# Optimization experiments

Measured on AMD Instinct MI355X. Metric: run time of the kernel, lower is better.

Reference implementation:

```python
import jax, jax.numpy as jnp
import numpy as np
import math

FACTOR = 5

def setup_inputs() -> dict:
    key = jax.random.key(0)
    k1, k2, k3, k4 = jax.random.split(key, 4)
    B, L, H, D = 4, 2048, 8, 64
    sample_k = FACTOR * math.ceil(math.log(L))  # 40
    queries = jax.random.normal(k1, (B, L, H, D), dtype=jnp.float32)
    keys = jax.random.normal(k2, (B, L, H, D), dtype=jnp.float32)
    values = jax.random.normal(k3, (B, L, H, D), dtype=jnp.float32)
    index_sample = jax.random.randint(k4, (L, sample_k), 0, L, dtype=jnp.int32)
    return {"queries": queries, "keys": keys, "values": values, "index_sample": index_sample}

def reference(queries, keys, values, index_sample):
    B, L_Q, H, D = queries.shape
    L_K = keys.shape[1]
    # [B,L,H,D] -> [B,H,L,D]
    Q = jnp.swapaxes(queries, 1, 2)
    K = jnp.swapaxes(keys, 1, 2)
    # values are cumsum'ed along the length axis before attention
    Vc = jnp.cumsum(jnp.swapaxes(values, 1, 2), axis=-2)
    u = min(FACTOR * math.ceil(math.log(L_Q)), L_Q)  # n_top
    # --- _prob_QK ---
    # gather sampled keys per query position: [B,H,L_Q,sample_k,D]
    K_sample = K[:, :, index_sample, :]
    # sampled scores: [B,H,L_Q,sample_k]
    Q_K_sample = jnp.einsum('bhqd,bhqsd->bhqs', Q, K_sample)
    # sparsity measure M = max - mean(scaled by L_K)
    M = Q_K_sample.max(axis=-1) - Q_K_sample.sum(axis=-1) / L_K  # [B,H,L_Q]
    M_top = jax.lax.top_k(M, u)[1]  # [B,H,u] query indices
    # gather top queries: [B,H,u,D]
    Q_reduce = jnp.take_along_axis(Q, M_top[..., None], axis=2)
    # full scores for selected queries: [B,H,u,L_K]
    scores = jnp.einsum('bhud,bhkd->bhuk', Q_reduce, K)
    scale = 1.0 / math.sqrt(D)
    scores = scores * scale
    # mask_flag=False, output_attention=False -> plain softmax then matmul with cumsum'ed V
    attn = jax.nn.softmax(scores, axis=-1)
    context = jnp.einsum('bhuk,bhkd->bhud', attn, Vc)  # [B,H,u,D]
    return context
```

## Files before the change

### kernel.cpp

```cpp
#include <hip/hip_runtime.h>
#include <hip/hip_bf16.h>
#include <math.h>

#define B 4
#define L 2048
#define H 8
#define D 64
#define SK 40
#define U 40
#define JC 32
#define JCL (L / JC)

#define OFF_M     0
#define OFF_TOP   262144
#define OFF_T     270336
#define OFF_PART  10756096
#define OFF_CSUM  21241856

__device__ __forceinline__ float dot4(float4 a, float4 b) {
    return fmaf(a.x, b.x, fmaf(a.y, b.y, fmaf(a.z, b.z, a.w * b.w)));
}

__global__ __launch_bounds__(256) void k_msamp(const float* __restrict__ Q,
                                               const float* __restrict__ K,
                                               const int* __restrict__ idx,
                                               float* __restrict__ M) {
    int g  = blockIdx.x & 7;
    int b  = g >> 1;
    int hh = g & 1;
    int t  = threadIdx.x;
    int wave = t >> 6;
    int lane = t & 63;
    int qp = lane >> 5;
    int hp = (lane >> 3) & 3;
    int c  = lane & 7;
    int h  = hh * 4 + hp;
    int q  = (blockIdx.x >> 3) * 8 + wave * 2 + qp;

    const float* qrow = Q + (size_t)((b * L + q) * H + h) * D + c * 8;
    float4 qa = *(const float4*)qrow;
    float4 qb = *(const float4*)(qrow + 4);

    int s1 = lane & 31;
    int v1 = idx[q * SK + s1];
    int s2 = 32 + s1; if (s2 > SK - 1) s2 = SK - 1;
    int v2 = idx[q * SK + s2];

    const float* kbase = K + (size_t)b * L * H * D + (size_t)h * D + c * 8;

    float vmax = -__builtin_inff();
    float vsum = 0.f;
#pragma unroll 8
    for (int s = 0; s < SK; ++s) {
        int kidx = (s < 32) ? __shfl(v1, qp * 32 + s, 64)
                            : __shfl(v2, qp * 32 + (s - 32), 64);
        const float* kp = kbase + (size_t)kidx * (H * D);
        float4 ka = *(const float4*)kp;
        float4 kb = *(const float4*)(kp + 4);
        float d8 = dot4(qa, ka) + dot4(qb, kb);
        d8 += __shfl_xor(d8, 1, 64);
        d8 += __shfl_xor(d8, 2, 64);
        d8 += __shfl_xor(d8, 4, 64);
        vmax = fmaxf(vmax, d8);
        vsum += d8;
    }
    if (c == 0) M[(size_t)(b * H + h) * L + q] = vmax - vsum * (1.0f / (float)L);
}

__global__ __launch_bounds__(256) void k_topk(const float* __restrict__ M,
                                              int* __restrict__ top) {
    __shared__ unsigned long long cand[L];
    __shared__ unsigned int bins[256];
    __shared__ unsigned int red[256];
    __shared__ int cnt2;

    int bh = blockIdx.x;
    int tid = threadIdx.x;
    const float* m = M + (size_t)bh * L;

    bins[tid] = 0;
    if (tid == 0) cnt2 = 0;

    const float4* m4 = (const float4*)(m + tid * 8);
    float4 fa = m4[0], fb = m4[1];
    float f8[8] = {fa.x, fa.y, fa.z, fa.w, fb.x, fb.y, fb.z, fb.w};
    unsigned int u8[8];
    unsigned int umin = 0xFFFFFFFFu, umax = 0u;
#pragma unroll
    for (int e = 0; e < 8; ++e) {
        unsigned int bits = __float_as_uint(f8[e]);
        unsigned int u = (bits & 0x80000000u) ? ~bits : (bits | 0x80000000u);
        u8[e] = u;
        umin = min(umin, u);
        umax = max(umax, u);
    }
    red[tid] = umin;
    __syncthreads();
    for (int s = 128; s; s >>= 1) {
        if (tid < s) red[tid] = min(red[tid], red[tid + s]);
        __syncthreads();
    }
    unsigned int kmin = red[0];
    __syncthreads();
    red[tid] = umax;
    __syncthreads();
    for (int s = 128; s; s >>= 1) {
        if (tid < s) red[tid] = max(red[tid], red[tid + s]);
        __syncthreads();
    }
    unsigned int kmax = red[0];
    __syncthreads();

    unsigned int range = kmax - kmin;
    if (range == 0u) {
        if (tid < U) top[bh * U + tid] = tid;
        return;
    }
    int hb = 31 - __clz(range);
    int shift = (hb > 7) ? (hb - 7) : 0;

#pragma unroll
    for (int e = 0; e < 8; ++e) {
        unsigned int bin = (u8[e] - kmin) >> shift;
        atomicAdd(&bins[bin], 1u);
    }
    __syncthreads();

    red[tid] = bins[tid];
    __syncthreads();
    for (int s = 1; s < 256; s <<= 1) {
        unsigned int add = (tid + s < 256) ? red[tid + s] : 0u;
        __syncthreads();
        red[tid] += add;
        __syncthreads();
    }
    int cnt = __syncthreads_count(red[tid] >= U);
    unsigned int t = (unsigned int)(cnt - 1);

#pragma unroll
    for (int e = 0; e < 8; ++e) {
        unsigned int u = u8[e];
        if (((u - kmin) >> shift) >= t) {
            int pos = atomicAdd(&cnt2, 1);
            int i = tid * 8 + e;
            cand[pos] = ((unsigned long long)u << 11) | (unsigned long long)(2047 - i);
        }
    }
    __syncthreads();
    int C = cnt2;

    for (int j = tid; j < C; j += 256) {
        unsigned long long kj = cand[j];
        int r = 0;
        for (int kk = 0; kk < C; ++kk) r += (cand[kk] > kj);
        if (r < U) top[bh * U + r] = 2047 - (int)(kj & 0x7FFull);
    }
}

__global__ __launch_bounds__(256) void k_scores(const float* __restrict__ Q,
                                                const float* __restrict__ K,
                                                const int* __restrict__ top,
                                                float* __restrict__ T,
                                                float* __restrict__ csum) {
    __shared__ float4 sQ4[U * 16];
    int bh = blockIdx.x >> 4;
    int kc = blockIdx.x & 15;
    int b = bh >> 3, h = bh & (H - 1);
    int tid = threadIdx.x;
    int lane = tid & 63;
    int w = tid >> 6;

    for (int i = tid; i < U * 16; i += 256) {
        int u = i >> 4, c = i & 15;
        int qidx = top[bh * U + u];
        sQ4[i] = *((const float4*)(Q + (size_t)((b * L + qidx) * H + h) * D) + c);
    }

    int k0 = kc * 128 + lane;
    const float4* kr0 = (const float4*)(K + (size_t)((b * L + k0) * H + h) * D);
    const float4* kr1 = (const float4*)(K + (size_t)((b * L + k0 + 64) * H + h) * D);
    float4 kv0[16], kv1[16];
#pragma unroll
    for (int i = 0; i < 16; ++i) { kv0[i] = kr0[i]; kv1[i] = kr1[i]; }
    __syncthreads();

    float* Tb = T + (size_t)bh * U * L;
    for (int uu = 0; uu < 10; ++uu) {
        int u = w * 10 + uu;
        float s0 = 0.f, s1 = 0.f;
#pragma unroll
        for (int i = 0; i < 16; ++i) {
            float4 q4 = sQ4[u * 16 + i];
            s0 += dot4(q4, kv0[i]);
            s1 += dot4(q4, kv1[i]);
        }
        float e0 = __expf(s0 * 0.125f);
        float e1 = __expf(s1 * 0.125f);
        Tb[(size_t)u * L + k0]      = e0;
        Tb[(size_t)u * L + k0 + 64] = e1;
        float c0 = e0, c1 = e1;
#pragma unroll
        for (int o = 1; o < 64; o <<= 1) {
            c0 += __shfl_xor(c0, o, 64);
            c1 += __shfl_xor(c1, o, 64);
        }
        if (lane == 0) {
            csum[((size_t)bh * U + u) * JC + 2 * kc]     = c0;
            csum[((size_t)bh * U + u) * JC + 2 * kc + 1] = c1;
        }
    }
}

__global__ __launch_bounds__(256) void k_ctx(const float* __restrict__ V,
                                             const float* __restrict__ E,
                                             const float* __restrict__ csum,
                                             float* __restrict__ part) {
    __shared__ float sT[U][JCL];
    int bh = blockIdx.x >> 5;
    int jc = blockIdx.x & 31;
    int b = bh >> 3, h = bh & (H - 1);
    int tid = threadIdx.x;
    int w = tid >> 6;
    int lane = tid & 63;
    int j2 = lane >> 4;
    int d4 = lane & 15;
    int jlane = lane & 31;

    const float* Eg = E + (size_t)bh * U * L + jc * JCL;
#pragma unroll
    for (int r = 0; r < 10; ++r) {
        int u = w * 10 + r;
        float cv = csum[((size_t)bh * U + u) * JC + jlane];
        float tv = (jlane > jc) ? cv : 0.f;
        tv += __shfl_xor(tv, 1, 64);
        tv += __shfl_xor(tv, 2, 64);
        tv += __shfl_xor(tv, 4, 64);
        tv += __shfl_xor(tv, 8, 64);
        tv += __shfl_xor(tv, 16, 64);
        float v = Eg[(size_t)u * L + lane];
#pragma unroll
        for (int s = 1; s < 64; s <<= 1) {
            float o = __shfl_down(v, s, 64);
            v += (lane + s < 64) ? o : 0.f;
        }
        sT[u][lane] = v + tv;
    }
    __syncthreads();

    float4 acc[10];
#pragma unroll
    for (int uu = 0; uu < 10; ++uu) acc[uu] = make_float4(0.f, 0.f, 0.f, 0.f);

    const float* Vb = V + (size_t)(b * L) * (H * D) + (size_t)h * D + d4 * 4;
#pragma unroll 4
    for (int it = 0; it < JCL / 4; ++it) {
        int j = it * 4 + j2;
        float4 v4 = *(const float4*)(Vb + (size_t)(jc * JCL + j) * (H * D));
#pragma unroll
        for (int uu = 0; uu < 10; ++uu) {
            float tj = sT[w * 10 + uu][j];
            acc[uu].x = fmaf(tj, v4.x, acc[uu].x);
            acc[uu].y = fmaf(tj, v4.y, acc[uu].y);
            acc[uu].z = fmaf(tj, v4.z, acc[uu].z);
            acc[uu].w = fmaf(tj, v4.w, acc[uu].w);
        }
    }

    float* po = part + ((size_t)jc * (B * H) + bh) * (U * D);
#pragma unroll
    for (int uu = 0; uu < 10; ++uu) {
        float4 a = acc[uu];
        a.x += __shfl_xor(a.x, 16, 64); a.y += __shfl_xor(a.y, 16, 64);
        a.z += __shfl_xor(a.z, 16, 64); a.w += __shfl_xor(a.w, 16, 64);
        a.x += __shfl_xor(a.x, 32, 64); a.y += __shfl_xor(a.y, 32, 64);
        a.z += __shfl_xor(a.z, 32, 64); a.w += __shfl_xor(a.w, 32, 64);
        if (j2 == 0) *(float4*)(po + (w * 10 + uu) * D + d4 * 4) = a;
    }
}

__global__ __launch_bounds__(256) void k_red(const float* __restrict__ part,
                                             const float* __restrict__ csum,
                                             float* __restrict__ out) {
    __shared__ float sden[4];
    int o = blockIdx.x * 256 + threadIdx.x;
    int bh = o / (U * D);
    int rest = o - bh * (U * D);
    int u = rest >> 6;
    int tid = threadIdx.x;
    int ubase = ((blockIdx.x * 256) % (U * D)) >> 6;

    if (tid < 128) {
        int ul = tid >> 5, j = tid & 31;
        float v = csum[((size_t)bh * U + ubase + ul) * JC + j];
        v += __shfl_xor(v, 1, 64);
        v += __shfl_xor(v, 2, 64);
        v += __shfl_xor(v, 4, 64);
        v += __shfl_xor(v, 8, 64);
        v += __shfl_xor(v, 16, 64);
        if (j == 0) sden[ul] = v;
    }
    __syncthreads();

    float s = 0.f;
#pragma unroll
    for (int jc = 0; jc < JC; ++jc)
        s += part[(size_t)(jc * (B * H) + bh) * (U * D) + rest];
    out[o] = s / sden[u - ubase];
}

extern "C" void kernel_launch(void* const* d_in, const int* in_sizes, int n_in,
                              void* d_out, int out_size, void* d_ws, size_t ws_size,
                              hipStream_t stream) {
    const float* Q  = (const float*)d_in[0];
    const float* K  = (const float*)d_in[1];
    const float* V  = (const float*)d_in[2];
    const int* idx  = (const int*)d_in[3];
    float* out = (float*)d_out;

    float* M    = (float*)((char*)d_ws + OFF_M);
    int*   top  = (int*)  ((char*)d_ws + OFF_TOP);
    float* T    = (float*)((char*)d_ws + OFF_T);
    float* part = (float*)((char*)d_ws + OFF_PART);
    float* csum = (float*)((char*)d_ws + OFF_CSUM);

    k_msamp<<<(L / 8) * 8, 256, 0, stream>>>(Q, K, idx, M);
    k_topk<<<B * H, 256, 0, stream>>>(M, top);
    k_scores<<<B * H * 16, 256, 0, stream>>>(Q, K, top, T, csum);
    k_ctx<<<B * H * JC, 256, 0, stream>>>(V, T, csum, part);
    k_red<<<(B * H * U * D) / 256, 256, 0, stream>>>(part, csum, out);
}
```

Before: 150.7 us.

## Fuse scores, context and reduction into one cooperative kernel with grid syncs

Replaces the three tail kernels (scores, context, reduce) with a single cooperative kernel of 256 blocks that runs each phase and separates them with grid-wide syncs. Each block now handles two key chunks per phase, and the context split is halved from 32 to 16 chunks, which shrinks the partial buffer and the final reduction. The aim is to remove launch gaps and cut partial-sum traffic. In exchange, grid sync adds its own cost, and the smaller grid gives less parallelism per phase. A fallback path launches the three phases as separate kernels if the cooperative launch fails.

```diff
diff --git a/kernel.cpp b/kernel.cpp
--- a/kernel.cpp
+++ b/kernel.cpp
@@ -1,6 +1,8 @@
 #include <hip/hip_runtime.h>
-#include <hip/hip_bf16.h>
+#include <hip/hip_cooperative_groups.h>
 #include <math.h>
+
+namespace cg = cooperative_groups;
 
 #define B 4
 #define L 2048
@@ -8,14 +10,15 @@
 #define D 64
 #define SK 40
 #define U 40
-#define JC 32
+#define JC 16
 #define JCL (L / JC)
+#define CSG 32
 
 #define OFF_M     0
 #define OFF_TOP   262144
 #define OFF_T     270336
 #define OFF_PART  10756096
-#define OFF_CSUM  21241856
+#define OFF_CSUM  15998976
 
 __device__ __forceinline__ float dot4(float4 a, float4 b) {
     return fmaf(a.x, b.x, fmaf(a.y, b.y, fmaf(a.z, b.z, a.w * b.w)));
@@ -157,155 +160,211 @@
     }
 }
 
-__global__ __launch_bounds__(256) void k_scores(const float* __restrict__ Q,
-                                                const float* __restrict__ K,
-                                                const int* __restrict__ top,
-                                                float* __restrict__ T,
-                                                float* __restrict__ csum) {
-    __shared__ float4 sQ4[U * 16];
-    int bh = blockIdx.x >> 4;
-    int kc = blockIdx.x & 15;
+
+__device__ __forceinline__ void phaseA(const float* __restrict__ Q,
+                                       const float* __restrict__ K,
+                                       const int* __restrict__ top,
+                                       float* __restrict__ T,
+                                       float* __restrict__ csum,
+                                       float4* sQ4) {
+    int tid = threadIdx.x, lane = tid & 63, w = tid >> 6;
+    int bh = blockIdx.x >> 3;
+    int kc2 = blockIdx.x & 7;
     int b = bh >> 3, h = bh & (H - 1);
-    int tid = threadIdx.x;
-    int lane = tid & 63;
-    int w = tid >> 6;
 
     for (int i = tid; i < U * 16; i += 256) {
         int u = i >> 4, c = i & 15;
         int qidx = top[bh * U + u];
         sQ4[i] = *((const float4*)(Q + (size_t)((b * L + qidx) * H + h) * D) + c);
     }
-
-    int k0 = kc * 128 + lane;
-    const float4* kr0 = (const float4*)(K + (size_t)((b * L + k0) * H + h) * D);
-    const float4* kr1 = (const float4*)(K + (size_t)((b * L + k0 + 64) * H + h) * D);
-    float4 kv0[16], kv1[16];
-#pragma unroll
-    for (int i = 0; i < 16; ++i) { kv0[i] = kr0[i]; kv1[i] = kr1[i]; }
     __syncthreads();
 
     float* Tb = T + (size_t)bh * U * L;
-    for (int uu = 0; uu < 10; ++uu) {
-        int u = w * 10 + uu;
-        float s0 = 0.f, s1 = 0.f;
-#pragma unroll
-        for (int i = 0; i < 16; ++i) {
-            float4 q4 = sQ4[u * 16 + i];
-            s0 += dot4(q4, kv0[i]);
-            s1 += dot4(q4, kv1[i]);
-        }
-        float e0 = __expf(s0 * 0.125f);
-        float e1 = __expf(s1 * 0.125f);
-        Tb[(size_t)u * L + k0]      = e0;
-        Tb[(size_t)u * L + k0 + 64] = e1;
-        float c0 = e0, c1 = e1;
-#pragma unroll
-        for (int o = 1; o < 64; o <<= 1) {
-            c0 += __shfl_xor(c0, o, 64);
-            c1 += __shfl_xor(c1, o, 64);
-        }
-        if (lane == 0) {
-            csum[((size_t)bh * U + u) * JC + 2 * kc]     = c0;
-            csum[((size_t)bh * U + u) * JC + 2 * kc + 1] = c1;
-        }
-    }
-}
-
-__global__ __launch_bounds__(256) void k_ctx(const float* __restrict__ V,
-                                             const float* __restrict__ E,
-                                             const float* __restrict__ csum,
-                                             float* __restrict__ part) {
-    __shared__ float sT[U][JCL];
-    int bh = blockIdx.x >> 5;
-    int jc = blockIdx.x & 31;
+    for (int sub = 0; sub < 2; ++sub) {
+        int kc = kc2 * 2 + sub;
+        int k0 = kc * 128 + lane;
+        const float4* kr0 = (const float4*)(K + (size_t)((b * L + k0) * H + h) * D);
+        const float4* kr1 = (const float4*)(K + (size_t)((b * L + k0 + 64) * H + h) * D);
+        float4 kv0[16], kv1[16];
+#pragma unroll
+        for (int i = 0; i < 16; ++i) { kv0[i] = kr0[i]; kv1[i] = kr1[i]; }
+
+        for (int uu = 0; uu < 10; ++uu) {
+            int u = w * 10 + uu;
+            float s0 = 0.f, s1 = 0.f;
+#pragma unroll
+            for (int i = 0; i < 16; ++i) {
+                float4 q4 = sQ4[u * 16 + i];
+                s0 += dot4(q4, kv0[i]);
+                s1 += dot4(q4, kv1[i]);
+            }
+            float e0 = __expf(s0 * 0.125f);
+            float e1 = __expf(s1 * 0.125f);
+            Tb[(size_t)u * L + k0]      = e0;
+            Tb[(size_t)u * L + k0 + 64] = e1;
+            float c0 = e0, c1 = e1;
+#pragma unroll
+            for (int o = 1; o < 64; o <<= 1) {
+                c0 += __shfl_xor(c0, o, 64);
+                c1 += __shfl_xor(c1, o, 64);
+            }
+            if (lane == 0) {
+                csum[((size_t)bh * U + u) * CSG + 2 * kc]     = c0;
+                csum[((size_t)bh * U + u) * CSG + 2 * kc + 1] = c1;
+            }
+        }
+    }
+}
+
+__device__ __forceinline__ void phaseB(const float* __restrict__ V,
+                                       const float* __restrict__ T,
+                                       const float* __restrict__ csum,
+                                       float* __restrict__ part,
+                                       float* sT) {
+    int tid = threadIdx.x, lane = tid & 63, w = tid >> 6;
+    int bh = blockIdx.x >> 3;
+    int jc2 = blockIdx.x & 7;
     int b = bh >> 3, h = bh & (H - 1);
-    int tid = threadIdx.x;
-    int w = tid >> 6;
-    int lane = tid & 63;
     int j2 = lane >> 4;
     int d4 = lane & 15;
     int jlane = lane & 31;
 
-    const float* Eg = E + (size_t)bh * U * L + jc * JCL;
-#pragma unroll
-    for (int r = 0; r < 10; ++r) {
-        int u = w * 10 + r;
-        float cv = csum[((size_t)bh * U + u) * JC + jlane];
-        float tv = (jlane > jc) ? cv : 0.f;
-        tv += __shfl_xor(tv, 1, 64);
-        tv += __shfl_xor(tv, 2, 64);
-        tv += __shfl_xor(tv, 4, 64);
-        tv += __shfl_xor(tv, 8, 64);
-        tv += __shfl_xor(tv, 16, 64);
-        float v = Eg[(size_t)u * L + lane];
-#pragma unroll
-        for (int s = 1; s < 64; s <<= 1) {
-            float o = __shfl_down(v, s, 64);
-            v += (lane + s < 64) ? o : 0.f;
-        }
-        sT[u][lane] = v + tv;
-    }
-    __syncthreads();
-
-    float4 acc[10];
-#pragma unroll
-    for (int uu = 0; uu < 10; ++uu) acc[uu] = make_float4(0.f, 0.f, 0.f, 0.f);
-
-    const float* Vb = V + (size_t)(b * L) * (H * D) + (size_t)h * D + d4 * 4;
+    for (int sub = 0; sub < 2; ++sub) {
+        int jc = jc2 * 2 + sub;
+        if (sub) __syncthreads();
+        const float* Eg = T + (size_t)bh * U * L + jc * JCL;
+        for (int r = 0; r < 10; ++r) {
+            int u = w * 10 + r;
+            float cv = csum[((size_t)bh * U + u) * CSG + jlane];
+            float tv = (jlane > 2 * jc + 1) ? cv : 0.f;
+            tv += __shfl_xor(tv, 1, 64);
+            tv += __shfl_xor(tv, 2, 64);
+            tv += __shfl_xor(tv, 4, 64);
+            tv += __shfl_xor(tv, 8, 64);
+            tv += __shfl_xor(tv, 16, 64);
+            float el = Eg[(size_t)u * L + lane];
+            float eh = Eg[(size_t)u * L + 64 + lane];
+            float sh = eh;
+#pragma unroll
+            for (int s = 1; s < 64; s <<= 1) {
+                float o = __shfl_down(sh, s, 64);
+                sh += (lane + s < 64) ? o : 0.f;
+            }
+            float th = __shfl(sh, 0, 64);
+            float sl = el;
+#pragma unroll
+            for (int s = 1; s < 64; s <<= 1) {
+                float o = __shfl_down(sl, s, 64);
+                sl += (lane + s < 64) ? o : 0.f;
+            }
+            sT[u * JCL + lane]      = sl + th + tv;
+            sT[u * JCL + 64 + lane] = sh + tv;
+        }
+        __syncthreads();
+
+        float4 acc[10];
+#pragma unroll
+        for (int uu = 0; uu < 10; ++uu) acc[uu] = make_float4(0.f, 0.f, 0.f, 0.f);
+
+        const float* Vb = V + (size_t)(b * L) * (H * D) + (size_t)h * D + d4 * 4;
 #pragma unroll 4
-    for (int it = 0; it < JCL / 4; ++it) {
-        int j = it * 4 + j2;
-        float4 v4 = *(const float4*)(Vb + (size_t)(jc * JCL + j) * (H * D));
+        for (int it = 0; it < JCL / 4; ++it) {
+            int j = it * 4 + j2;
+            float4 v4 = *(const float4*)(Vb + (size_t)(jc * JCL + j) * (H * D));
+#pragma unroll
+            for (int uu = 0; uu < 10; ++uu) {
+                float tj = sT[(w * 10 + uu) * JCL + j];
+                acc[uu].x = fmaf(tj, v4.x, acc[uu].x);
+                acc[uu].y = fmaf(tj, v4.y, acc[uu].y);
+                acc[uu].z = fmaf(tj, v4.z, acc[uu].z);
+                acc[uu].w = fmaf(tj, v4.w, acc[uu].w);
+            }
+        }
+
+        float* po = part + ((size_t)jc * (B * H) + bh) * (U * D);
 #pragma unroll
         for (int uu = 0; uu < 10; ++uu) {
-            float tj = sT[w * 10 + uu][j];
-            acc[uu].x = fmaf(tj, v4.x, acc[uu].x);
-            acc[uu].y = fmaf(tj, v4.y, acc[uu].y);
-            acc[uu].z = fmaf(tj, v4.z, acc[uu].z);
-            acc[uu].w = fmaf(tj, v4.w, acc[uu].w);
-        }
-    }
-
-    float* po = part + ((size_t)jc * (B * H) + bh) * (U * D);
-#pragma unroll
-    for (int uu = 0; uu < 10; ++uu) {
-        float4 a = acc[uu];
-        a.x += __shfl_xor(a.x, 16, 64); a.y += __shfl_xor(a.y, 16, 64);
-        a.z += __shfl_xor(a.z, 16, 64); a.w += __shfl_xor(a.w, 16, 64);
-        a.x += __shfl_xor(a.x, 32, 64); a.y += __shfl_xor(a.y, 32, 64);
-        a.z += __shfl_xor(a.z, 32, 64); a.w += __shfl_xor(a.w, 32, 64);
-        if (j2 == 0) *(float4*)(po + (w * 10 + uu) * D + d4 * 4) = a;
-    }
-}
-
-__global__ __launch_bounds__(256) void k_red(const float* __restrict__ part,
-                                             const float* __restrict__ csum,
-                                             float* __restrict__ out) {
-    __shared__ float sden[4];
-    int o = blockIdx.x * 256 + threadIdx.x;
-    int bh = o / (U * D);
-    int rest = o - bh * (U * D);
-    int u = rest >> 6;
+            float4 a = acc[uu];
+            a.x += __shfl_xor(a.x, 16, 64); a.y += __shfl_xor(a.y, 16, 64);
+            a.z += __shfl_xor(a.z, 16, 64); a.w += __shfl_xor(a.w, 16, 64);
+            a.x += __shfl_xor(a.x, 32, 64); a.y += __shfl_xor(a.y, 32, 64);
+            a.z += __shfl_xor(a.z, 32, 64); a.w += __shfl_xor(a.w, 32, 64);
+            if (j2 == 0) *(float4*)(po + (w * 10 + uu) * D + d4 * 4) = a;
+        }
+    }
+}
+
+__device__ __forceinline__ void phaseC(const float* __restrict__ part,
+                                       const float* __restrict__ csum,
+                                       float* __restrict__ out,
+                                       float* sden) {
+    int bh = blockIdx.x;
+    if (bh >= B * H) return;
     int tid = threadIdx.x;
-    int ubase = ((blockIdx.x * 256) % (U * D)) >> 6;
-
-    if (tid < 128) {
-        int ul = tid >> 5, j = tid & 31;
-        float v = csum[((size_t)bh * U + ubase + ul) * JC + j];
+    int jlane = tid & 31;
+
+    for (int p = 0; p < 5; ++p) {
+        int u = p * 8 + (tid >> 5);
+        float v = csum[((size_t)bh * U + u) * CSG + jlane];
         v += __shfl_xor(v, 1, 64);
         v += __shfl_xor(v, 2, 64);
         v += __shfl_xor(v, 4, 64);
         v += __shfl_xor(v, 8, 64);
         v += __shfl_xor(v, 16, 64);
-        if (j == 0) sden[ul] = v;
-    }
-    __syncthreads();
-
-    float s = 0.f;
-#pragma unroll
-    for (int jc = 0; jc < JC; ++jc)
-        s += part[(size_t)(jc * (B * H) + bh) * (U * D) + rest];
-    out[o] = s / sden[u - ubase];
+        if (jlane == 0) sden[u] = v;
+    }
+    __syncthreads();
+
+    const float* pb = part + (size_t)bh * (U * D);
+    float* ob = out + (size_t)bh * (U * D);
+    for (int it = 0; it < 10; ++it) {
+        int rest = it * 256 + tid;
+        int u = rest >> 6;
+        float s = 0.f;
+#pragma unroll
+        for (int jc = 0; jc < JC; ++jc)
+            s += pb[(size_t)jc * (B * H) * (U * D) + rest];
+        ob[rest] = s / sden[u];
+    }
+}
+
+__global__ __launch_bounds__(256, 2) void k_tail(const float* __restrict__ Q,
+                                                 const float* __restrict__ K,
+                                                 const int* __restrict__ top,
+                                                 const float* __restrict__ V,
+                                                 float* __restrict__ T,
+                                                 float* __restrict__ csum,
+                                                 float* __restrict__ part,
+                                                 float* __restrict__ out) {
+    __shared__ __align__(16) char smem[U * JCL * 4];
+    cg::grid_group grid = cg::this_grid();
+    phaseA(Q, K, top, T, csum, (float4*)smem);
+    grid.sync();
+    phaseB(V, T, csum, part, (float*)smem);
+    grid.sync();
+    phaseC(part, csum, out, (float*)smem);
+}
+
+__global__ __launch_bounds__(256) void k_phA(const float* __restrict__ Q,
+                                             const float* __restrict__ K,
+                                             const int* __restrict__ top,
+                                             float* __restrict__ T,
+                                             float* __restrict__ csum) {
+    __shared__ __align__(16) char smem[U * 16 * 16];
+    phaseA(Q, K, top, T, csum, (float4*)smem);
+}
+__global__ __launch_bounds__(256) void k_phB(const float* __restrict__ V,
+                                             const float* __restrict__ T,
+                                             const float* __restrict__ csum,
+                                             float* __restrict__ part) {
+    __shared__ __align__(16) char smem[U * JCL * 4];
+    phaseB(V, T, csum, part, (float*)smem);
+}
+__global__ __launch_bounds__(256) void k_phC(const float* __restrict__ part,
+                                             const float* __restrict__ csum,
+                                             float* __restrict__ out) {
+    __shared__ float sden[U];
+    phaseC(part, csum, out, sden);
 }
 
 extern "C" void kernel_launch(void* const* d_in, const int* in_sizes, int n_in,
@@ -325,7 +384,14 @@
 
     k_msamp<<<(L / 8) * 8, 256, 0, stream>>>(Q, K, idx, M);
     k_topk<<<B * H, 256, 0, stream>>>(M, top);
-    k_scores<<<B * H * 16, 256, 0, stream>>>(Q, K, top, T, csum);
-    k_ctx<<<B * H * JC, 256, 0, stream>>>(V, T, csum, part);
-    k_red<<<(B * H * U * D) / 256, 256, 0, stream>>>(part, csum, out);
-}
+
+    void* args[] = {(void*)&Q, (void*)&K, (void*)&top, (void*)&V,
+                    (void*)&T, (void*)&csum, (void*)&part, (void*)&out};
+    hipError_t e = hipLaunchCooperativeKernel((const void*)k_tail, dim3(256),
+                                              dim3(256), args, 0, stream);
+    if (e != hipSuccess) {
+        k_phA<<<256, 256, 0, stream>>>(Q, K, top, T, csum);
+        k_phB<<<256, 256, 0, stream>>>(V, T, csum, part);
+        k_phC<<<B * H, 256, 0, stream>>>(part, csum, out);
+    }
+}
```

Result: slower. 228.4 us (+51.5%).

## Rebalance score and context kernels to 512-thread blocks with 16 key chunks

Applied to the files above, without the earlier changes.

The score kernel now uses 512 threads, each holding one key row instead of two, with the 40 selected queries split across four thread groups. The context kernel uses 16 key chunks of 128 instead of 32 chunks of 64, and 512 threads with five queries per wave. Each wave now does two chained prefix scans per query row. This halves the partial-sum buffer and the reduction work in k_red while changing register pressure and occupancy. The blocks are larger but there are half as many in the context kernel, so fewer workgroups are available to hide latency.

```diff
diff --git a/kernel.cpp b/kernel.cpp
--- a/kernel.cpp
+++ b/kernel.cpp
@@ -1,5 +1,4 @@
 #include <hip/hip_runtime.h>
-#include <hip/hip_bf16.h>
 #include <math.h>
 
 #define B 4
@@ -8,14 +7,15 @@
 #define D 64
 #define SK 40
 #define U 40
-#define JC 32
+#define JC 16
 #define JCL (L / JC)
+#define CSG 32
 
 #define OFF_M     0
 #define OFF_TOP   262144
 #define OFF_T     270336
 #define OFF_PART  10756096
-#define OFF_CSUM  21241856
+#define OFF_CSUM  15998976
 
 __device__ __forceinline__ float dot4(float4 a, float4 b) {
     return fmaf(a.x, b.x, fmaf(a.y, b.y, fmaf(a.z, b.z, a.w * b.w)));
@@ -157,99 +157,100 @@
     }
 }
 
-__global__ __launch_bounds__(256) void k_scores(const float* __restrict__ Q,
+
+__global__ __launch_bounds__(512, 4) void k_phA(const float* __restrict__ Q,
                                                 const float* __restrict__ K,
                                                 const int* __restrict__ top,
                                                 float* __restrict__ T,
                                                 float* __restrict__ csum) {
-    __shared__ float4 sQ4[U * 16];
+    __shared__ __align__(16) float4 sQ4[U * 16];
+    int tid = threadIdx.x;
     int bh = blockIdx.x >> 4;
     int kc = blockIdx.x & 15;
     int b = bh >> 3, h = bh & (H - 1);
-    int tid = threadIdx.x;
-    int lane = tid & 63;
-    int w = tid >> 6;
-
-    for (int i = tid; i < U * 16; i += 256) {
+
+    for (int i = tid; i < U * 16; i += 512) {
         int u = i >> 4, c = i & 15;
         int qidx = top[bh * U + u];
         sQ4[i] = *((const float4*)(Q + (size_t)((b * L + qidx) * H + h) * D) + c);
     }
 
-    int k0 = kc * 128 + lane;
-    const float4* kr0 = (const float4*)(K + (size_t)((b * L + k0) * H + h) * D);
-    const float4* kr1 = (const float4*)(K + (size_t)((b * L + k0 + 64) * H + h) * D);
-    float4 kv0[16], kv1[16];
-#pragma unroll
-    for (int i = 0; i < 16; ++i) { kv0[i] = kr0[i]; kv1[i] = kr1[i]; }
+    int ugrp   = tid >> 7;
+    int colgrp = tid & 127;
+    int col = kc * 128 + colgrp;
+
+    const float4* kr = (const float4*)(K + (size_t)((b * L + col) * H + h) * D);
+    float4 kv[16];
+#pragma unroll
+    for (int i = 0; i < 16; ++i) kv[i] = kr[i];
     __syncthreads();
 
     float* Tb = T + (size_t)bh * U * L;
+    int cs = 2 * kc + (colgrp >> 6);
+#pragma unroll
     for (int uu = 0; uu < 10; ++uu) {
-        int u = w * 10 + uu;
-        float s0 = 0.f, s1 = 0.f;
-#pragma unroll
-        for (int i = 0; i < 16; ++i) {
-            float4 q4 = sQ4[u * 16 + i];
-            s0 += dot4(q4, kv0[i]);
-            s1 += dot4(q4, kv1[i]);
-        }
-        float e0 = __expf(s0 * 0.125f);
-        float e1 = __expf(s1 * 0.125f);
-        Tb[(size_t)u * L + k0]      = e0;
-        Tb[(size_t)u * L + k0 + 64] = e1;
-        float c0 = e0, c1 = e1;
-#pragma unroll
-        for (int o = 1; o < 64; o <<= 1) {
-            c0 += __shfl_xor(c0, o, 64);
-            c1 += __shfl_xor(c1, o, 64);
-        }
-        if (lane == 0) {
-            csum[((size_t)bh * U + u) * JC + 2 * kc]     = c0;
-            csum[((size_t)bh * U + u) * JC + 2 * kc + 1] = c1;
-        }
-    }
-}
-
-__global__ __launch_bounds__(256) void k_ctx(const float* __restrict__ V,
-                                             const float* __restrict__ E,
-                                             const float* __restrict__ csum,
-                                             float* __restrict__ part) {
-    __shared__ float sT[U][JCL];
-    int bh = blockIdx.x >> 5;
-    int jc = blockIdx.x & 31;
+        int u = ugrp * 10 + uu;
+        float s = 0.f;
+#pragma unroll
+        for (int i = 0; i < 16; ++i) s += dot4(sQ4[u * 16 + i], kv[i]);
+        float e = __expf(s * 0.125f);
+        Tb[(size_t)u * L + col] = e;
+        float c0 = e;
+#pragma unroll
+        for (int o = 1; o < 64; o <<= 1) c0 += __shfl_xor(c0, o, 64);
+        if ((colgrp & 63) == 0) csum[((size_t)bh * U + u) * CSG + cs] = c0;
+    }
+}
+
+__global__ __launch_bounds__(512, 4) void k_phB(const float* __restrict__ V,
+                                                const float* __restrict__ T,
+                                                const float* __restrict__ csum,
+                                                float* __restrict__ part) {
+    __shared__ __align__(16) float sT[U * JCL];
+    int tid = threadIdx.x;
+    int bh = blockIdx.x >> 4;
+    int jc = blockIdx.x & 15;
     int b = bh >> 3, h = bh & (H - 1);
-    int tid = threadIdx.x;
-    int w = tid >> 6;
+    int w8   = tid >> 6;
     int lane = tid & 63;
+
     int j2 = lane >> 4;
     int d4 = lane & 15;
     int jlane = lane & 31;
 
-    const float* Eg = E + (size_t)bh * U * L + jc * JCL;
-#pragma unroll
-    for (int r = 0; r < 10; ++r) {
-        int u = w * 10 + r;
-        float cv = csum[((size_t)bh * U + u) * JC + jlane];
-        float tv = (jlane > jc) ? cv : 0.f;
+    const float* Eg = T + (size_t)bh * U * L + jc * JCL;
+    for (int r = 0; r < 5; ++r) {
+        int u = w8 * 5 + r;
+        float cv = csum[((size_t)bh * U + u) * CSG + jlane];
+        float tv = (jlane > 2 * jc + 1) ? cv : 0.f;
         tv += __shfl_xor(tv, 1, 64);
         tv += __shfl_xor(tv, 2, 64);
         tv += __shfl_xor(tv, 4, 64);
         tv += __shfl_xor(tv, 8, 64);
         tv += __shfl_xor(tv, 16, 64);
-        float v = Eg[(size_t)u * L + lane];
+        float el = Eg[(size_t)u * L + lane];
+        float eh = Eg[(size_t)u * L + 64 + lane];
+        float sh = eh;
 #pragma unroll
         for (int s = 1; s < 64; s <<= 1) {
-            float o = __shfl_down(v, s, 64);
-            v += (lane + s < 64) ? o : 0.f;
+            float o = __shfl_down(sh, s, 64);
+            sh += (lane + s < 64) ? o : 0.f;
         }
-        sT[u][lane] = v + tv;
-    }
-    __syncthreads();
-
-    float4 acc[10];
-#pragma unroll
-    for (int uu = 0; uu < 10; ++uu) acc[uu] = make_float4(0.f, 0.f, 0.f, 0.f);
+        float th = __shfl(sh, 0, 64);
+        float sl = el;
+#pragma unroll
+        for (int s = 1; s < 64; s <<= 1) {
+            float o = __shfl_down(sl, s, 64);
+            sl += (lane + s < 64) ? o : 0.f;
+        }
+        sT[u * JCL + lane]      = sl + th + tv;
+        sT[u * JCL + 64 + lane] = sh + tv;
+    }
+    __syncthreads();
+
+    float4 acc[5];
+#pragma unroll
+    for (int uu = 0; uu < 5; ++uu) acc[uu] = make_float4(0.f, 0.f, 0.f, 0.f);
 
     const float* Vb = V + (size_t)(b * L) * (H * D) + (size_t)h * D + d4 * 4;
 #pragma unroll 4
@@ -257,8 +258,8 @@
         int j = it * 4 + j2;
         float4 v4 = *(const float4*)(Vb + (size_t)(jc * JCL + j) * (H * D));
 #pragma unroll
-        for (int uu = 0; uu < 10; ++uu) {
-            float tj = sT[w * 10 + uu][j];
+        for (int uu = 0; uu < 5; ++uu) {
+            float tj = sT[(w8 * 5 + uu) * JCL + j];
             acc[uu].x = fmaf(tj, v4.x, acc[uu].x);
             acc[uu].y = fmaf(tj, v4.y, acc[uu].y);
             acc[uu].z = fmaf(tj, v4.z, acc[uu].z);
@@ -268,13 +269,13 @@
 
     float* po = part + ((size_t)jc * (B * H) + bh) * (U * D);
 #pragma unroll
-    for (int uu = 0; uu < 10; ++uu) {
+    for (int uu = 0; uu < 5; ++uu) {
         float4 a = acc[uu];
         a.x += __shfl_xor(a.x, 16, 64); a.y += __shfl_xor(a.y, 16, 64);
         a.z += __shfl_xor(a.z, 16, 64); a.w += __shfl_xor(a.w, 16, 64);
         a.x += __shfl_xor(a.x, 32, 64); a.y += __shfl_xor(a.y, 32, 64);
         a.z += __shfl_xor(a.z, 32, 64); a.w += __shfl_xor(a.w, 32, 64);
-        if (j2 == 0) *(float4*)(po + (w * 10 + uu) * D + d4 * 4) = a;
+        if (j2 == 0) *(float4*)(po + (w8 * 5 + uu) * D + d4 * 4) = a;
     }
 }
 
@@ -291,7 +292,7 @@
 
     if (tid < 128) {
         int ul = tid >> 5, j = tid & 31;
-        float v = csum[((size_t)bh * U + ubase + ul) * JC + j];
+        float v = csum[((size_t)bh * U + ubase + ul) * CSG + j];
         v += __shfl_xor(v, 1, 64);
         v += __shfl_xor(v, 2, 64);
         v += __shfl_xor(v, 4, 64);
@@ -325,7 +326,7 @@
 
     k_msamp<<<(L / 8) * 8, 256, 0, stream>>>(Q, K, idx, M);
     k_topk<<<B * H, 256, 0, stream>>>(M, top);
-    k_scores<<<B * H * 16, 256, 0, stream>>>(Q, K, top, T, csum);
-    k_ctx<<<B * H * JC, 256, 0, stream>>>(V, T, csum, part);
+    k_phA<<<B * H * 16, 512, 0, stream>>>(Q, K, top, T, csum);
+    k_phB<<<B * H * 16, 512, 0, stream>>>(V, T, csum, part);
     k_red<<<(B * H * U * D) / 256, 256, 0, stream>>>(part, csum, out);
 }
```

New measurement: 144.0 us. -4.5%, faster.
